# Optimization experiments

Measured on AMD Instinct MI355X. Metric: run time of the kernel, lower is better.

Reference implementation:

```python
import jax, jax.numpy as jnp
import numpy as np
from math import sqrt

N = 8192
INPUT_SIZE = 256
D_MODEL = 256


def setup_inputs() -> dict:
    key = jax.random.key(0)
    k1, k2, k3, k4 = jax.random.split(key, 4)
    x = jax.random.normal(k1, (N, INPUT_SIZE), dtype=jnp.float32)
    adj = jax.random.randint(k2, (N, N), 0, 2, dtype=jnp.int32)
    # torch nn.Linear(input_size, d_model): weight [d_model, input_size], bias [d_model]
    bound = 1.0 / sqrt(INPUT_SIZE)
    Vw = jax.random.uniform(k3, (D_MODEL, INPUT_SIZE), dtype=jnp.float32, minval=-bound, maxval=bound)
    Vb = jax.random.uniform(k4, (D_MODEL,), dtype=jnp.float32, minval=-bound, maxval=bound)
    return {"x": x, "adj": adj, "Vw": Vw, "Vb": Vb}


def reference(x, adj, Vw, Vb):
    # value = V(x)
    value = x @ Vw.T + Vb                                  # [N, d_model]
    # scores = x x^T / sqrt(d_model), masked where adj == 0
    scores = (x @ x.T) * (1.0 / sqrt(D_MODEL))             # [N, N]
    scores = jnp.where(adj == 0, jnp.float32(-1e9), scores)
    p_attn = jax.nn.softmax(scores, axis=-1)               # [N, N]
    Vs = p_attn @ value                                    # [N, d_model]
    return (Vs, p_attn)
```

## Files before the change

### kernel.cpp

```cpp
#include <hip/hip_runtime.h>
#include <hip/hip_bf16.h>


#define NN 8192
#define DD 256

typedef __attribute__((ext_vector_type(8))) short bf16x8;
typedef __attribute__((ext_vector_type(8))) unsigned short u16x8;
typedef __attribute__((ext_vector_type(4))) float f32x4;
typedef __attribute__((ext_vector_type(4))) int i32x4;

__device__ __forceinline__ unsigned short f2bf(float f) {
  unsigned u = __builtin_bit_cast(unsigned, f);
  u += 0x7fffu + ((u >> 16) & 1u);
  return (unsigned short)(u >> 16);
}
__device__ __forceinline__ float bf2f(unsigned short h) {
  unsigned u = ((unsigned)h) << 16;
  return __builtin_bit_cast(float, u);
}
__device__ __forceinline__ unsigned pack2(float a, float b) {
  return (unsigned)f2bf(a) | ((unsigned)f2bf(b) << 16);
}

__global__ void k_prep_x(const float* __restrict__ x, unsigned short* __restrict__ xb) {
  int t = blockIdx.x * 256 + threadIdx.x;
  const float4* s = reinterpret_cast<const float4*>(x) + (size_t)t * 2;
  float4 f0 = s[0], f1 = s[1];
  uint4 o;
  o.x = pack2(f0.x, f0.y); o.y = pack2(f0.z, f0.w);
  o.z = pack2(f1.x, f1.y); o.w = pack2(f1.z, f1.w);
  reinterpret_cast<uint4*>(xb)[t] = o;
}

__global__ void k_prep_adj(const int* __restrict__ adj, unsigned char* __restrict__ adjp) {
  size_t t = (size_t)blockIdx.x * 256 + threadIdx.x;
  const i32x4* s = reinterpret_cast<const i32x4*>(adj) + t * 2;
  i32x4 v0 = __builtin_nontemporal_load(s);
  i32x4 v1 = __builtin_nontemporal_load(s + 1);
  unsigned b = 0;
  b |= (v0[0] != 0) ? 1u : 0u;  b |= (v0[1] != 0) ? 2u : 0u;
  b |= (v0[2] != 0) ? 4u : 0u;  b |= (v0[3] != 0) ? 8u : 0u;
  b |= (v1[0] != 0) ? 16u : 0u; b |= (v1[1] != 0) ? 32u : 0u;
  b |= (v1[2] != 0) ? 64u : 0u; b |= (v1[3] != 0) ? 128u : 0u;
  adjp[t] = (unsigned char)b;
}

__global__ __launch_bounds__(256) void k_value(
    const float* __restrict__ Vw, const float* __restrict__ Vb,
    const unsigned short* __restrict__ xb, unsigned short* __restrict__ vT) {
  __shared__ unsigned short lB[64 * 256];
  int mb = blockIdx.x >> 2, nb = blockIdx.x & 3;
  int tid = threadIdx.x, lane = tid & 63, w = tid >> 6;
  int mw = w >> 1, nw = w & 1;
  {
    int n_l = tid >> 2, q = tid & 3;
#pragma unroll
    for (int o = 0; o < 8; ++o) {
      int k0 = q * 64 + o * 8;
      const float4* src = reinterpret_cast<const float4*>(Vw + (nb * 64 + n_l) * DD + k0);
      float4 g0 = src[0], g1 = src[1];
      uint4 pk;
      pk.x = pack2(g0.x, g0.y); pk.y = pack2(g0.z, g0.w);
      pk.z = pack2(g1.x, g1.y); pk.w = pack2(g1.z, g1.w);
      *reinterpret_cast<uint4*>(reinterpret_cast<char*>(lB) + n_l * 512 + ((k0 * 2) ^ ((n_l & 7) << 4))) = pk;
    }
  }
  bf16x8 aR[2][8];
#pragma unroll
  for (int mf = 0; mf < 2; ++mf) {
    int rg = mb * 64 + mw * 32 + mf * 16 + (lane & 15);
    const char* base = reinterpret_cast<const char*>(xb + (size_t)rg * DD);
#pragma unroll
    for (int ks = 0; ks < 8; ++ks)
      aR[mf][ks] = *reinterpret_cast<const bf16x8*>(base + ks * 64 + ((lane >> 4) * 16));
  }
  __syncthreads();
  f32x4 acc[2][2] = {};
#pragma unroll
  for (int ks = 0; ks < 8; ++ks) {
    int kb = ks * 64 + ((lane >> 4) * 16);
#pragma unroll
    for (int nf = 0; nf < 2; ++nf) {
      int n = nw * 32 + nf * 16 + (lane & 15);
      bf16x8 b = *reinterpret_cast<const bf16x8*>(reinterpret_cast<const char*>(lB) + n * 512 + (kb ^ ((n & 7) << 4)));
#pragma unroll
      for (int mf = 0; mf < 2; ++mf)
        acc[mf][nf] = __builtin_amdgcn_mfma_f32_16x16x32_bf16(aR[mf][ks], b, acc[mf][nf], 0, 0, 0);
    }
  }
#pragma unroll
  for (int nf = 0; nf < 2; ++nf) {
    int n_g = nb * 64 + nw * 32 + nf * 16 + (lane & 15);
    float vb = Vb[n_g];
#pragma unroll
    for (int mf = 0; mf < 2; ++mf) {
      int m_g = mb * 64 + mw * 32 + mf * 16 + ((lane >> 4) << 2);
      ushort4 h;
      h.x = f2bf(acc[mf][nf][0] + vb);
      h.y = f2bf(acc[mf][nf][1] + vb);
      h.z = f2bf(acc[mf][nf][2] + vb);
      h.w = f2bf(acc[mf][nf][3] + vb);
      *reinterpret_cast<ushort4*>(vT + (size_t)n_g * NN + m_g) = h;
    }
  }
}

__global__ __launch_bounds__(512, 4) void k_pass1(
    const unsigned short* __restrict__ xb, const unsigned long long* __restrict__ adjp,
    unsigned short* __restrict__ ews, float* __restrict__ lpart) {
  __shared__ char lB[2][32768];
  int cs = blockIdx.x >> 6, rb = blockIdx.x & 63;
  int tid = threadIdx.x, lane = tid & 63, w = tid >> 6;
  int ln = lane & 15, kq = lane >> 4;
  int colb = cs * 1024;
  int r0 = rb * 128 + w * 16 + (kq << 2);

  bf16x8 aR[8];
  {
    const char* abase = reinterpret_cast<const char*>(xb + (size_t)(rb * 128 + w * 16 + ln) * DD);
#pragma unroll
    for (int ks = 0; ks < 8; ++ks)
      aR[ks] = *reinterpret_cast<const bf16x8*>(abase + ks * 64 + kq * 16);
  }

#define LOADB(G, KC)                                                                   \
  _Pragma("unroll") for (int q = 0; q < 4; ++q) {                                      \
    int id_ = q * 512 + tid, col_ = id_ >> 5, oct_ = id_ & 31;                         \
    (G)[q] = *reinterpret_cast<const uint4*>(xb + (size_t)(colb + (KC) * 64 + col_) * DD + oct_ * 8); \
  }
#define DSWRITE(G, BB)                                                                 \
  _Pragma("unroll") for (int q = 0; q < 4; ++q) {                                      \
    int id_ = q * 512 + tid, col_ = id_ >> 5, oct_ = id_ & 31;                         \
    *reinterpret_cast<uint4*>(&lB[BB][col_ * 512 + ((oct_ * 16) ^ ((col_ & 7) << 4))]) = (G)[q]; \
  }

  uint4 gB[4];
  LOADB(gB, 0);
  DSWRITE(gB, 0);
  __syncthreads();

  float rsum[4] = {};
  for (int kc = 0; kc < 16; ++kc) {
    bool has = kc < 15;
    if (has) LOADB(gB, kc + 1);
    unsigned long long m[4];
#pragma unroll
    for (int i = 0; i < 4; ++i)
      m[i] = adjp[(size_t)(r0 + i) * 128 + cs * 16 + kc];
    const char* bufc = lB[kc & 1];
    f32x4 acc[4] = {};
#pragma unroll
    for (int ks = 0; ks < 8; ++ks) {
      int kb = ks * 64 + kq * 16;
#pragma unroll
      for (int nf = 0; nf < 4; ++nf) {
        int cc = nf * 16 + ln;
        bf16x8 b = *reinterpret_cast<const bf16x8*>(bufc + cc * 512 + (kb ^ ((cc & 7) << 4)));
        acc[nf] = __builtin_amdgcn_mfma_f32_16x16x32_bf16(aR[ks], b, acc[nf], 0, 0, 0);
      }
    }
    int c0 = colb + kc * 64 + ln;
#pragma unroll
    for (int nf = 0; nf < 4; ++nf)
#pragma unroll
      for (int i = 0; i < 4; ++i) {
        bool on = (m[i] >> (nf * 16 + ln)) & 1;
        float e = on ? __expf(acc[nf][i] * 0.0625f) : 0.f;
        unsigned short h = f2bf(e);
        ews[(size_t)(r0 + i) * NN + c0 + nf * 16] = h;
        rsum[i] += bf2f(h);
      }
    if (has) DSWRITE(gB, (kc + 1) & 1);
    __syncthreads();
  }
#pragma unroll
  for (int i = 0; i < 4; ++i) {
    float r = rsum[i];
    r += __shfl_xor(r, 1); r += __shfl_xor(r, 2);
    r += __shfl_xor(r, 4); r += __shfl_xor(r, 8);
    if (ln == 0) lpart[(size_t)cs * NN + r0 + i] = r;
  }
#undef LOADB
#undef DSWRITE
}

__global__ void k_reduce_l(const float* __restrict__ lpart, float* __restrict__ rl) {
  int i = blockIdx.x * 256 + threadIdx.x;
  float s = 0.f;
  for (int c = 0; c < 8; ++c) s += lpart[(size_t)c * NN + i];
  rl[i] = s > 0.f ? 1.f / s : 0.f;
}

__global__ __launch_bounds__(512) void k_vs(
    const unsigned short* __restrict__ ews, const unsigned short* __restrict__ vT,
    const float* __restrict__ rl, unsigned short* __restrict__ vspb) {
  __shared__ char lV[2][65536];
  int rt = blockIdx.x >> 2, ck = blockIdx.x & 3;
  int tid = threadIdx.x, lane = tid & 63, w = tid >> 6;
  int ln = lane & 15, kq = lane >> 4;
  int row = rt * 128 + w * 16 + ln;
  const unsigned short* ap = ews + (size_t)row * NN + ck * 2048 + kq * 8;

#define LOADB(G, KC)                                                                     \
  _Pragma("unroll") for (int q = 0; q < 8; ++q) {                                        \
    int id_ = q * 512 + tid, n_ = id_ >> 4, o_ = id_ & 15;                               \
    (G)[q] = *reinterpret_cast<const uint4*>(vT + (size_t)n_ * NN + ck * 2048 + (KC) * 128 + o_ * 8); \
  }
#define DSWRITE(G, BB)                                                                   \
  _Pragma("unroll") for (int q = 0; q < 8; ++q) {                                        \
    int id_ = q * 512 + tid, n_ = id_ >> 4, o_ = id_ & 15;                               \
    *reinterpret_cast<uint4*>(&lV[BB][n_ * 256 + ((o_ * 16) ^ ((n_ & 7) << 4))]) = (G)[q]; \
  }
#define LOADA(A, KC)                                                                     \
  _Pragma("unroll") for (int s_ = 0; s_ < 4; ++s_)                                       \
    (A)[s_] = __builtin_nontemporal_load(reinterpret_cast<const bf16x8*>(ap + (KC) * 128 + s_ * 32));

  uint4 gB[8];
  bf16x8 aC[4], aN[4];
  LOADB(gB, 0);
  LOADA(aC, 0);
  DSWRITE(gB, 0);
  __syncthreads();

  f32x4 acc[16] = {};
  for (int kc = 0; kc < 16; ++kc) {
    bool has = kc < 15;
    if (has) {
      LOADB(gB, kc + 1);
      LOADA(aN, kc + 1);
    }
    const char* bufc = lV[kc & 1];
#pragma unroll
    for (int ks = 0; ks < 4; ++ks) {
#pragma unroll
      for (int nf = 0; nf < 16; ++nf) {
        int n = nf * 16 + ln;
        bf16x8 b = *reinterpret_cast<const bf16x8*>(bufc + n * 256 + ((ks * 64 + kq * 16) ^ ((n & 7) << 4)));
        acc[nf] = __builtin_amdgcn_mfma_f32_16x16x32_bf16(aC[ks], b, acc[nf], 0, 0, 0);
      }
    }
    if (has) DSWRITE(gB, (kc + 1) & 1);
    __syncthreads();
#pragma unroll
    for (int s = 0; s < 4; ++s) aC[s] = aN[s];
  }

  int rowo = rt * 128 + w * 16 + kq * 4;
#pragma unroll
  for (int i = 0; i < 4; ++i) {
    float rli = rl[rowo + i];
#pragma unroll
    for (int nf = 0; nf < 16; ++nf) {
      int n = nf * 16 + ln;
      vspb[((size_t)ck * NN + rowo + i) * DD + n] = f2bf(acc[nf][i] * rli);
    }
  }
#undef LOADB
#undef DSWRITE
#undef LOADA
}

__global__ void k_norm(const unsigned short* __restrict__ ews, const float* __restrict__ rl,
                       float* __restrict__ pout) {
  size_t t = (size_t)blockIdx.x * 256 + threadIdx.x;
  float r = rl[t >> 10];
  u16x8 v = __builtin_nontemporal_load(reinterpret_cast<const u16x8*>(ews + t * 8));
  f32x4 o0, o1;
  o0[0] = bf2f(v[0]) * r; o0[1] = bf2f(v[1]) * r; o0[2] = bf2f(v[2]) * r; o0[3] = bf2f(v[3]) * r;
  o1[0] = bf2f(v[4]) * r; o1[1] = bf2f(v[5]) * r; o1[2] = bf2f(v[6]) * r; o1[3] = bf2f(v[7]) * r;
  f32x4* pd = reinterpret_cast<f32x4*>(pout + t * 8);
  __builtin_nontemporal_store(o0, pd);
  __builtin_nontemporal_store(o1, pd + 1);
}

__global__ void k_reduce_vs(const unsigned short* __restrict__ vspb, float* __restrict__ vout) {
  int t = blockIdx.x * 256 + threadIdx.x;
  float s[8] = {};
#pragma unroll
  for (int c = 0; c < 4; ++c) {
    u16x8 v = *reinterpret_cast<const u16x8*>(vspb + (size_t)c * NN * DD + (size_t)t * 8);
#pragma unroll
    for (int j = 0; j < 8; ++j) s[j] += bf2f(v[j]);
  }
  float4 o0, o1;
  o0.x = s[0]; o0.y = s[1]; o0.z = s[2]; o0.w = s[3];
  o1.x = s[4]; o1.y = s[5]; o1.z = s[6]; o1.w = s[7];
  float4* d = reinterpret_cast<float4*>(vout + (size_t)t * 8);
  d[0] = o0; d[1] = o1;
}

extern "C" void kernel_launch(void* const* d_in, const int* in_sizes, int n_in,
                              void* d_out, int out_size, void* d_ws, size_t ws_size,
                              hipStream_t stream) {
  const float* x   = (const float*)d_in[0];
  const int*   adj = (const int*)d_in[1];
  const float* Vw  = (const float*)d_in[2];
  const float* Vb  = (const float*)d_in[3];
  float* out   = (float*)d_out;
  float* vs_out = out;
  float* p_out  = out + (size_t)NN * DD;
  char* ws = (char*)d_ws;
  unsigned short* xb   = (unsigned short*)(ws);
  unsigned short* vT   = (unsigned short*)(ws + ((size_t)4  << 20));
  float* rl            = (float*)(ws + ((size_t)8  << 20));
  float* lpart         = (float*)(ws + ((size_t)9  << 20));
  unsigned short* vspb = (unsigned short*)(ws + ((size_t)11 << 20));
  unsigned short* ews  = (unsigned short*)(ws + ((size_t)27 << 20));
  unsigned char* adjp  = (unsigned char*)(ws + ((size_t)156 << 20));

  k_prep_x<<<dim3(1024), dim3(256), 0, stream>>>(x, xb);
  k_prep_adj<<<dim3(32768), dim3(256), 0, stream>>>(adj, adjp);
  k_value<<<dim3(512), dim3(256), 0, stream>>>(Vw, Vb, xb, vT);
  k_pass1<<<dim3(512), dim3(512), 0, stream>>>(xb, (const unsigned long long*)adjp, ews, lpart);
  k_reduce_l<<<dim3(32), dim3(256), 0, stream>>>(lpart, rl);
  k_vs<<<dim3(256), dim3(512), 0, stream>>>(ews, vT, rl, vspb);
  k_norm<<<dim3(32768), dim3(256), 0, stream>>>(ews, rl, p_out);
  k_reduce_vs<<<dim3(1024), dim3(256), 0, stream>>>(vspb, vs_out);
}
```

Baseline: 320.9 us.

## Restructure pass1 to keep column tile in LDS and stream row tiles

The QK^T/exp pass is reorganized so each 256-thread block loads one 64-column B tile into LDS once and then streams 16 row tiles of A from global memory into registers, with double-buffered register prefetch of A and the mask. This removes the per-iteration LDS refill and the block-wide barriers inside the loop. The catch is 128 column partitions of row sums, so the row-sum reduction now reads 128 partials per row, and lpart is moved to a larger workspace region that overlaps vspb. That overlap is safe only because k_reduce_l runs before k_vs writes vspb.

Result: slower. 572.8 us (+78.5%).

```diff
diff --git a/kernel.cpp b/kernel.cpp
--- a/kernel.cpp
+++ b/kernel.cpp
@@ -106,49 +106,47 @@
   }
 }
 
-__global__ __launch_bounds__(512, 4) void k_pass1(
+__global__ __launch_bounds__(256, 4) void k_pass1(
     const unsigned short* __restrict__ xb, const unsigned long long* __restrict__ adjp,
     unsigned short* __restrict__ ews, float* __restrict__ lpart) {
-  __shared__ char lB[2][32768];
-  int cs = blockIdx.x >> 6, rb = blockIdx.x & 63;
+  __shared__ char lB[32768];
+  int cb = blockIdx.x & 127, rs = blockIdx.x >> 7;
   int tid = threadIdx.x, lane = tid & 63, w = tid >> 6;
   int ln = lane & 15, kq = lane >> 4;
-  int colb = cs * 1024;
-  int r0 = rb * 128 + w * 16 + (kq << 2);
-
-  bf16x8 aR[8];
-  {
-    const char* abase = reinterpret_cast<const char*>(xb + (size_t)(rb * 128 + w * 16 + ln) * DD);
-#pragma unroll
-    for (int ks = 0; ks < 8; ++ks)
-      aR[ks] = *reinterpret_cast<const bf16x8*>(abase + ks * 64 + kq * 16);
-  }
-
-#define LOADB(G, KC)                                                                   \
-  _Pragma("unroll") for (int q = 0; q < 4; ++q) {                                      \
-    int id_ = q * 512 + tid, col_ = id_ >> 5, oct_ = id_ & 31;                         \
-    (G)[q] = *reinterpret_cast<const uint4*>(xb + (size_t)(colb + (KC) * 64 + col_) * DD + oct_ * 8); \
-  }
-#define DSWRITE(G, BB)                                                                 \
-  _Pragma("unroll") for (int q = 0; q < 4; ++q) {                                      \
-    int id_ = q * 512 + tid, col_ = id_ >> 5, oct_ = id_ & 31;                         \
-    *reinterpret_cast<uint4*>(&lB[BB][col_ * 512 + ((oct_ * 16) ^ ((col_ & 7) << 4))]) = (G)[q]; \
-  }
-
-  uint4 gB[4];
-  LOADB(gB, 0);
-  DSWRITE(gB, 0);
+#pragma unroll
+  for (int q = 0; q < 8; ++q) {
+    int id = q * 256 + tid, col = id >> 5, oct = id & 31;
+    uint4 v = *reinterpret_cast<const uint4*>(xb + (size_t)(cb * 64 + col) * DD + oct * 8);
+    *reinterpret_cast<uint4*>(&lB[col * 512 + ((oct * 16) ^ ((col & 7) << 4))]) = v;
+  }
   __syncthreads();
-
-  float rsum[4] = {};
-  for (int kc = 0; kc < 16; ++kc) {
-    bool has = kc < 15;
-    if (has) LOADB(gB, kc + 1);
-    unsigned long long m[4];
-#pragma unroll
-    for (int i = 0; i < 4; ++i)
-      m[i] = adjp[(size_t)(r0 + i) * 128 + cs * 16 + kc];
-    const char* bufc = lB[kc & 1];
+  int c0 = cb * 64 + ln;
+
+#define LOADA(A, IT)                                                                    \
+  {                                                                                     \
+    const char* ab_ = reinterpret_cast<const char*>(                                    \
+        xb + (size_t)(rs * 1024 + (IT) * 64 + w * 16 + ln) * DD);                       \
+    _Pragma("unroll") for (int ks_ = 0; ks_ < 8; ++ks_)                                 \
+      (A)[ks_] = *reinterpret_cast<const bf16x8*>(ab_ + ks_ * 64 + kq * 16);            \
+  }
+#define LOADM(M, IT)                                                                    \
+  {                                                                                     \
+    int rm_ = rs * 1024 + (IT) * 64 + w * 16 + kq * 4;                                  \
+    _Pragma("unroll") for (int i_ = 0; i_ < 4; ++i_)                                    \
+      (M)[i_] = adjp[(size_t)(rm_ + i_) * 128 + cb];                                    \
+  }
+
+  bf16x8 aC[8], aN[8];
+  unsigned long long mC[4], mN[4];
+  LOADA(aC, 0);
+  LOADM(mC, 0);
+
+  for (int it = 0; it < 16; ++it) {
+    bool has = it < 15;
+    if (has) {
+      LOADA(aN, it + 1);
+      LOADM(mN, it + 1);
+    }
     f32x4 acc[4] = {};
 #pragma unroll
     for (int ks = 0; ks < 8; ++ks) {
@@ -156,39 +154,42 @@
 #pragma unroll
       for (int nf = 0; nf < 4; ++nf) {
         int cc = nf * 16 + ln;
-        bf16x8 b = *reinterpret_cast<const bf16x8*>(bufc + cc * 512 + (kb ^ ((cc & 7) << 4)));
-        acc[nf] = __builtin_amdgcn_mfma_f32_16x16x32_bf16(aR[ks], b, acc[nf], 0, 0, 0);
+        bf16x8 b = *reinterpret_cast<const bf16x8*>(&lB[cc * 512 + (kb ^ ((cc & 7) << 4))]);
+        acc[nf] = __builtin_amdgcn_mfma_f32_16x16x32_bf16(aC[ks], b, acc[nf], 0, 0, 0);
       }
     }
-    int c0 = colb + kc * 64 + ln;
+    int r0 = rs * 1024 + it * 64 + w * 16 + kq * 4;
+    float rsum[4] = {};
 #pragma unroll
     for (int nf = 0; nf < 4; ++nf)
 #pragma unroll
       for (int i = 0; i < 4; ++i) {
-        bool on = (m[i] >> (nf * 16 + ln)) & 1;
+        bool on = (mC[i] >> (nf * 16 + ln)) & 1;
         float e = on ? __expf(acc[nf][i] * 0.0625f) : 0.f;
         unsigned short h = f2bf(e);
         ews[(size_t)(r0 + i) * NN + c0 + nf * 16] = h;
         rsum[i] += bf2f(h);
       }
-    if (has) DSWRITE(gB, (kc + 1) & 1);
-    __syncthreads();
-  }
-#pragma unroll
-  for (int i = 0; i < 4; ++i) {
-    float r = rsum[i];
-    r += __shfl_xor(r, 1); r += __shfl_xor(r, 2);
-    r += __shfl_xor(r, 4); r += __shfl_xor(r, 8);
-    if (ln == 0) lpart[(size_t)cs * NN + r0 + i] = r;
-  }
-#undef LOADB
-#undef DSWRITE
+#pragma unroll
+    for (int i = 0; i < 4; ++i) {
+      float r = rsum[i];
+      r += __shfl_xor(r, 1); r += __shfl_xor(r, 2);
+      r += __shfl_xor(r, 4); r += __shfl_xor(r, 8);
+      if (ln == 0) lpart[(size_t)cb * NN + r0 + i] = r;
+    }
+#pragma unroll
+    for (int s = 0; s < 8; ++s) aC[s] = aN[s];
+#pragma unroll
+    for (int i = 0; i < 4; ++i) mC[i] = mN[i];
+  }
+#undef LOADA
+#undef LOADM
 }
 
 __global__ void k_reduce_l(const float* __restrict__ lpart, float* __restrict__ rl) {
   int i = blockIdx.x * 256 + threadIdx.x;
   float s = 0.f;
-  for (int c = 0; c < 8; ++c) s += lpart[(size_t)c * NN + i];
+  for (int c = 0; c < 128; ++c) s += lpart[(size_t)c * NN + i];
   rl[i] = s > 0.f ? 1.f / s : 0.f;
 }
 
@@ -304,7 +305,7 @@
   unsigned short* xb   = (unsigned short*)(ws);
   unsigned short* vT   = (unsigned short*)(ws + ((size_t)4  << 20));
   float* rl            = (float*)(ws + ((size_t)8  << 20));
-  float* lpart         = (float*)(ws + ((size_t)9  << 20));
+  float* lpart         = (float*)(ws + ((size_t)11 << 20));
   unsigned short* vspb = (unsigned short*)(ws + ((size_t)11 << 20));
   unsigned short* ews  = (unsigned short*)(ws + ((size_t)27 << 20));
   unsigned char* adjp  = (unsigned char*)(ws + ((size_t)156 << 20));
@@ -312,7 +313,7 @@
   k_prep_x<<<dim3(1024), dim3(256), 0, stream>>>(x, xb);
   k_prep_adj<<<dim3(32768), dim3(256), 0, stream>>>(adj, adjp);
   k_value<<<dim3(512), dim3(256), 0, stream>>>(Vw, Vb, xb, vT);
-  k_pass1<<<dim3(512), dim3(512), 0, stream>>>(xb, (const unsigned long long*)adjp, ews, lpart);
+  k_pass1<<<dim3(1024), dim3(256), 0, stream>>>(xb, (const unsigned long long*)adjp, ews, lpart);
   k_reduce_l<<<dim3(32), dim3(256), 0, stream>>>(lpart, rl);
   k_vs<<<dim3(256), dim3(512), 0, stream>>>(ews, vT, rl, vspb);
   k_norm<<<dim3(32768), dim3(256), 0, stream>>>(ews, rl, p_out);
```
